# Kernel tuning notes

Measured on AMD Instinct MI355X. Metric: run time of the kernel, lower is better.

The kernel has to match this reference:

```python
import jax, jax.numpy as jnp
import numpy as np

B, T_SRC, T_TGT = 2048, 32, 32
D = 512            # d_model
D_SRC, D_TGT = 100, 80
L = 2              # n_layers


def setup_inputs() -> dict:
    key = jax.random.key(0)
    ks = jax.random.split(key, 16)
    s = 1.0 / float(np.sqrt(D))  # torch LSTM init scale
    u = lambda k, shape: jax.random.uniform(k, shape, jnp.float32, -s, s)
    return {
        "src": jax.random.randint(ks[0], (B, T_SRC), 0, D_SRC, dtype=jnp.int32),
        "tgt": jax.random.randint(ks[1], (B, T_TGT), 0, D_TGT, dtype=jnp.int32),
        "enc_emb": jax.random.normal(ks[2], (D_SRC, D), jnp.float32),
        "dec_emb": jax.random.normal(ks[3], (D_TGT, D), jnp.float32),
        "enc_Wih": u(ks[4], (L, 4 * D, D)),
        "enc_Whh": u(ks[5], (L, 4 * D, D)),
        "enc_bih": u(ks[6], (L, 4 * D)),
        "enc_bhh": u(ks[7], (L, 4 * D)),
        "dec_Wih": u(ks[8], (L, 4 * D, D)),
        "dec_Whh": u(ks[9], (L, 4 * D, D)),
        "dec_bih": u(ks[10], (L, 4 * D)),
        "dec_bhh": u(ks[11], (L, 4 * D)),
        "post_W": u(ks[12], (D_TGT, D)),
        "post_b": u(ks[13], (D_TGT,)),
    }


def lstm_cell(x, h, c, Wih, Whh, bih, bhh):
    # PyTorch gate order: i, f, g, o
    gates = x @ Wih.T + bih + h @ Whh.T + bhh  # [B, 4D]
    i, f, g, o = jnp.split(gates, 4, axis=-1)
    c_new = jax.nn.sigmoid(f) * c + jax.nn.sigmoid(i) * jnp.tanh(g)
    h_new = jax.nn.sigmoid(o) * jnp.tanh(c_new)
    return h_new, c_new


def reference(src, tgt, enc_emb, dec_emb, enc_Wih, enc_Whh, enc_bih, enc_bhh,
              dec_Wih, dec_Whh, dec_bih, dec_bhh, post_W, post_b):
    # Eval-mode forward: dropout = identity, teacher forcing disabled
    # (tf = random() < ratio AND self.training is False at inference).
    n_layers = enc_Wih.shape[0]
    Bb = src.shape[0]
    Dm = enc_emb.shape[1]

    # ---- encoder: multi-layer LSTM over src embeddings ----
    x = enc_emb[src].swapaxes(0, 1)  # [T_src, B, D]
    hs, cs = [], []
    z = jnp.zeros((Bb, Dm), x.dtype)
    for l in range(n_layers):
        def step(carry, xt, l=l):
            h, c = carry
            h, c = lstm_cell(xt, h, c, enc_Wih[l], enc_Whh[l], enc_bih[l], enc_bhh[l])
            return (h, c), h
        (hT, cT), x = jax.lax.scan(step, (z, z), x)
        hs.append(hT)
        cs.append(cT)
    h0 = jnp.stack(hs)  # [L, B, D]
    c0 = jnp.stack(cs)  # [L, B, D]

    prev0 = dec_emb[tgt[:, 0]]  # [B, D]

    def dec_step(carry, _):
        h, c, prev = carry
        x = prev
        new_h, new_c = [], []
        for l in range(n_layers):
            hl, cl = lstm_cell(x, h[l], c[l], dec_Wih[l], dec_Whh[l], dec_bih[l], dec_bhh[l])
            new_h.append(hl)
            new_c.append(cl)
            x = hl
        logits = x @ post_W.T + post_b          # [B, d_tgt]
        pred = jnp.argmax(logits, axis=-1)       # [B]
        prev = dec_emb[pred]                     # [B, D]
        return (jnp.stack(new_h), jnp.stack(new_c), prev), logits

    _, out = jax.lax.scan(dec_step, (h0, c0, prev0), None, length=tgt.shape[1])
    return out.swapaxes(0, 1)  # [B, T_tgt, d_tgt]
```

## Files before the change

### kernel.cpp

```cpp
#include <hip/hip_runtime.h>
#include <hip/hip_bf16.h>

#define B_  2048
#define T_  32
#define D_  512
#define G_  2048
#define VT_ 80
#define BD  (B_ * D_)
#define LWE ((size_t)G_ * D_)

typedef _Float16 half8 __attribute__((ext_vector_type(8)));
typedef _Float16 half4_t __attribute__((ext_vector_type(4)));
typedef float    f32x4 __attribute__((ext_vector_type(4)));

static __device__ __forceinline__ float sigm(float x) {
    return 1.0f / (1.0f + expf(-x));
}

__global__ void zero_ws(int4* __restrict__ p, int n) {
    int i = blockIdx.x * blockDim.x + threadIdx.x;
    if (i < n) p[i] = int4{0, 0, 0, 0};
}
__global__ void init_pred(const int* __restrict__ tgt, int* __restrict__ pred) {
    int i = blockIdx.x * blockDim.x + threadIdx.x;
    if (i < B_) pred[i] = tgt[i * T_];
}

__global__ void split_weights(const float* __restrict__ s0, const float* __restrict__ s1,
                              const float* __restrict__ s2, const float* __restrict__ s3,
                              const float* __restrict__ s4, const float* __restrict__ s5,
                              _Float16* __restrict__ Wbase) {
    int g = blockIdx.x * blockDim.x + threadIdx.x;
    int mat = g >> 17;
    int rem = g & 131071;
    int np  = rem >> 6;
    int kq  = rem & 63;
    const float* src = (mat == 0) ? s0 : (mat == 1) ? s1 : (mat == 2) ? s2
                     : (mat == 3) ? s3 : (mat == 4) ? s4 : s5;
    int n = (np & 3) * D_ + (np >> 2);
    const float* sp = src + (size_t)n * D_ + kq * 8;
    float4 v0 = ((const float4*)sp)[0], v1 = ((const float4*)sp)[1];
    float x[8] = {v0.x, v0.y, v0.z, v0.w, v1.x, v1.y, v1.z, v1.w};
    _Float16 hi[8], lo[8];
    #pragma unroll
    for (int u = 0; u < 8; ++u) {
        hi[u] = (_Float16)x[u];
        lo[u] = (_Float16)(x[u] - (float)hi[u]);
    }
    int tile = (np >> 4) * 16 + (kq >> 2);
    int lane = (np & 15) | ((kq & 3) << 4);
    size_t e = (size_t)tile * 512 + (size_t)lane * 8;
    _Float16* Whi = Wbase + (size_t)mat * (2 * LWE);
    _Float16* Wlo = Whi + LWE;
    *(half8*)(Whi + e) = *(half8*)hi;
    *(half8*)(Wlo + e) = *(half8*)lo;
}

__global__ void split_postW(const float* __restrict__ pw,
                            _Float16* __restrict__ Ph, _Float16* __restrict__ Pl) {
    int g = blockIdx.x * blockDim.x + threadIdx.x;
    if (g >= VT_ * 64) return;
    int v = g >> 6, kq = g & 63;
    const float* sp = pw + (size_t)v * D_ + kq * 8;
    float4 v0 = ((const float4*)sp)[0], v1 = ((const float4*)sp)[1];
    float x[8] = {v0.x, v0.y, v0.z, v0.w, v1.x, v1.y, v1.z, v1.w};
    _Float16 hi[8], lo[8];
    #pragma unroll
    for (int u = 0; u < 8; ++u) {
        hi[u] = (_Float16)x[u];
        lo[u] = (_Float16)(x[u] - (float)hi[u]);
    }
    int tile = (v >> 4) * 16 + (kq >> 2);
    int lane = (v & 15) | ((kq & 3) << 4);
    size_t e = (size_t)tile * 512 + (size_t)lane * 8;
    *(half8*)(Ph + e) = *(half8*)hi;
    *(half8*)(Pl + e) = *(half8*)lo;
}

__global__ void perm_bias(const float* __restrict__ ebih, const float* __restrict__ ebhh,
                          const float* __restrict__ dbih, const float* __restrict__ dbhh,
                          float* __restrict__ biasP) {
    int i = blockIdx.x * blockDim.x + threadIdx.x;
    int cfg = i >> 11, np = i & 2047;
    int n = (np & 3) * D_ + (np >> 2);
    const float* bi = ((cfg < 2) ? ebih : dbih) + (cfg & 1) * G_;
    const float* bh = ((cfg < 2) ? ebhh : dbhh) + (cfg & 1) * G_;
    biasP[cfg * G_ + np] = bi[n] + bh[n];
}

__global__ __launch_bounds__(256) void compute_P(
    const float* __restrict__ enc_emb, const float* __restrict__ dec_emb,
    const float* __restrict__ encW0,   const float* __restrict__ decW0,
    float* __restrict__ P) {
    __shared__ float es[10][D_];
    __shared__ float part[4][64][10];
    int by = blockIdx.y;
    bool enc = (by < 10);
    int r0 = enc ? by * 10 : 100 + (by - 10) * 10;
    int s0 = enc ? by * 10 : (by - 10) * 10;
    const float* emb = enc ? enc_emb : dec_emb;
    const float* W   = enc ? encW0 : decW0;
    int tid = threadIdx.x;
    #pragma unroll
    for (int it = 0; it < 5; ++it) {
        int i4 = it * 256 + tid;
        int rr = i4 >> 7, cc = i4 & 127;
        ((float4*)es[rr])[cc] = ((const float4*)(emb + (size_t)(s0 + rr) * D_))[cc];
    }
    __syncthreads();
    int o   = tid & 63;
    int seg = tid >> 6;
    int np = blockIdx.x * 64 + o;
    int n = (np & 3) * D_ + (np >> 2);
    const float* wr = W + (size_t)n * D_ + seg * 128;
    float acc[10];
    #pragma unroll
    for (int rr = 0; rr < 10; ++rr) acc[rr] = 0.f;
    for (int k = 0; k < 128; k += 4) {
        float4 w4 = *(const float4*)(wr + k);
        int kb = seg * 128 + k;
        #pragma unroll
        for (int rr = 0; rr < 10; ++rr)
            acc[rr] += es[rr][kb] * w4.x + es[rr][kb+1] * w4.y
                     + es[rr][kb+2] * w4.z + es[rr][kb+3] * w4.w;
    }
    #pragma unroll
    for (int rr = 0; rr < 10; ++rr) part[seg][o][rr] = acc[rr];
    __syncthreads();
    for (int i = tid; i < 640; i += 256) {
        int o2 = i & 63, rr = i >> 6;
        P[(size_t)(r0 + rr) * G_ + blockIdx.x * 64 + o2] =
            (part[0][o2][rr] + part[1][o2][rr]) + (part[2][o2][rr] + part[3][o2][rr]);
    }
}

static __device__ __forceinline__ void load_chunk(
    const _Float16* __restrict__ Ah, const _Float16* __restrict__ Al,
    const _Float16* __restrict__ Wh, const _Float16* __restrict__ Wl,
    int afr, int wfr, int kc, int lane, half8* A8, half8* B8) {
    size_t lo8 = (size_t)lane * 8;
    #pragma unroll
    for (int i = 0; i < 4; ++i) {
        size_t off = (((size_t)(afr + i) * 16 + kc) << 9) + lo8;
        A8[i]     = *(const half8*)(Ah + off);
        A8[4 + i] = *(const half8*)(Al + off);
    }
    #pragma unroll
    for (int j = 0; j < 4; ++j) {
        size_t off = (((size_t)(wfr + j) * 16 + kc) << 9) + lo8;
        B8[j]     = *(const half8*)(Wh + off);
        B8[4 + j] = *(const half8*)(Wl + off);
    }
}
static __device__ __forceinline__ void mfma_chunk(
    const half8* A8, const half8* B8, f32x4 acc[4][4]) {
    #pragma unroll
    for (int i = 0; i < 4; ++i)
        #pragma unroll
        for (int j = 0; j < 4; ++j) {
            acc[i][j] = __builtin_amdgcn_mfma_f32_16x16x32_f16(A8[i], B8[j], acc[i][j], 0, 0, 0);
            acc[i][j] = __builtin_amdgcn_mfma_f32_16x16x32_f16(A8[i], B8[4 + j], acc[i][j], 0, 0, 0);
            acc[i][j] = __builtin_amdgcn_mfma_f32_16x16x32_f16(A8[4 + i], B8[j], acc[i][j], 0, 0, 0);
        }
}

struct CellJob {
    const _Float16 *a0h, *a0l, *w0h, *w0l;
    int kclo0, kchi0;
    const _Float16 *a1h, *a1l, *w1h, *w1l;
    int kclo1, kchi1;
    const float *biasP;
    const float *P;
    const int  *idx;
    int idx_stride, emb_rows;
    float *c_io;
    _Float16 *hh_out, *hl_out;
};

__global__ __launch_bounds__(512, 2) void lstm_cell_mfma(CellJob J0, CellJob J1) {
    const CellJob J = (blockIdx.z == 0) ? J0 : J1;
    __shared__ float gf[128][68];
    const int tid  = threadIdx.x;
    const int w    = tid >> 6;
    const int lane = tid & 63;
    const int g    = w >> 2;
    const int mw   = w & 3;
    const int bx   = blockIdx.x;
    const int m0   = blockIdx.y * 256;

    const _Float16* Ah = g ? J.a1h : J.a0h;
    const _Float16* Al = g ? J.a1l : J.a0l;
    const _Float16* Wh = g ? J.w1h : J.w0h;
    const _Float16* Wl = g ? J.w1l : J.w0l;
    const int kclo = g ? J.kclo1 : J.kclo0;
    const int kchi = g ? J.kchi1 : J.kchi0;

    const int afr = (m0 >> 4) + mw * 4;
    const int wfr = bx * 4;

    f32x4 acc[4][4];
    #pragma unroll
    for (int i = 0; i < 4; ++i)
        #pragma unroll
        for (int j = 0; j < 4; ++j) acc[i][j] = f32x4{0.f, 0.f, 0.f, 0.f};

    half8 A0[8], B0[8], A1[8], B1[8];
    load_chunk(Ah, Al, Wh, Wl, afr, wfr, kclo, lane, A0, B0);
    for (int kc = kclo; kc < kchi; kc += 2) {
        load_chunk(Ah, Al, Wh, Wl, afr, wfr, kc + 1, lane, A1, B1);
        mfma_chunk(A0, B0, acc);
        if (kc + 2 < kchi)
            load_chunk(Ah, Al, Wh, Wl, afr, wfr, kc + 2, lane, A0, B0);
        mfma_chunk(A1, B1, acc);
    }

    const int rbase = (lane >> 4) << 2;
    const int cbase = lane & 15;
    for (int p = 0; p < 2; ++p) {
        if (g == 0 && (mw >> 1) == p) {
            #pragma unroll
            for (int i = 0; i < 4; ++i) {
                int mrow = (mw & 1) * 64 + i * 16 + rbase;
                #pragma unroll
                for (int j = 0; j < 4; ++j) {
                    int nc = j * 16 + cbase;
                    #pragma unroll
                    for (int r = 0; r < 4; ++r)
                        gf[mrow + r][nc] = acc[i][j][r];
                }
            }
        }
        __syncthreads();
        if (g == 1 && (mw >> 1) == p) {
            #pragma unroll
            for (int i = 0; i < 4; ++i) {
                int mrow = (mw & 1) * 64 + i * 16 + rbase;
                #pragma unroll
                for (int j = 0; j < 4; ++j) {
                    int nc = j * 16 + cbase;
                    #pragma unroll
                    for (int r = 0; r < 4; ++r)
                        gf[mrow + r][nc] += acc[i][j][r];
                }
            }
        }
        __syncthreads();
        {
            int mr = tid >> 2, q = tid & 3;
            int mg = m0 + p * 128 + mr;
            const float4* brow = (const float4*)(J.biasP + (bx << 6));
            const float4* Pr = nullptr;
            if (J.P) {
                int s = J.idx[mg * J.idx_stride];
                s = min(max(s, 0), J.emb_rows - 1);
                Pr = (const float4*)(J.P + (size_t)s * G_ + (bx << 6));
            }
            float* crow = J.c_io + (size_t)mg * D_ + (bx << 4) + (q << 2);
            float4 cv = *(float4*)crow;
            _Float16 hh4[4], hl4[4];
            #pragma unroll
            for (int e = 0; e < 4; ++e) {
                int dl = (q << 2) + e;
                float4 g4 = *(float4*)&gf[mr][dl << 2];
                float4 b4 = brow[dl];
                float gi = g4.x + b4.x, gF = g4.y + b4.y;
                float gg = g4.z + b4.z, go = g4.w + b4.w;
                if (Pr) {
                    float4 p4 = Pr[dl];
                    gi += p4.x; gF += p4.y; gg += p4.z; go += p4.w;
                }
                float cc = (&cv.x)[e];
                float cn = sigm(gF) * cc + sigm(gi) * tanhf(gg);
                float hn = sigm(go) * tanhf(cn);
                (&cv.x)[e] = cn;
                _Float16 hH = (_Float16)hn;
                hh4[e] = hH;
                hl4[e] = (_Float16)(hn - (float)hH);
            }
            *(float4*)crow = cv;
            int kk = (bx << 4) + (q << 2);
            size_t hoff = ((size_t)((mg >> 4) * 16 + (kk >> 5)) << 9)
                        + (size_t)((mg & 15) | (((kk >> 3) & 3) << 4)) * 8
                        + ((q & 1) << 2);
            *(half4_t*)(J.hh_out + hoff) = *(half4_t*)hh4;
            *(half4_t*)(J.hl_out + hoff) = *(half4_t*)hl4;
        }
        __syncthreads();
    }
}

__global__ __launch_bounds__(128) void logits_mfma(
    const _Float16* __restrict__ Ah, const _Float16* __restrict__ Al,
    const _Float16* __restrict__ Bh, const _Float16* __restrict__ Bl,
    const float* __restrict__ postb, float* __restrict__ out,
    int t, int* __restrict__ pred) {
    __shared__ float gf2[64][85];
    __shared__ float pb[VT_];
    const int tid = threadIdx.x;
    const int w = tid >> 6;
    const int lane = tid & 63;
    const int m0 = blockIdx.x * 64;
    const int afr = blockIdx.x * 4;

    f32x4 acc[4][5];
    #pragma unroll
    for (int i = 0; i < 4; ++i)
        #pragma unroll
        for (int j = 0; j < 5; ++j) acc[i][j] = f32x4{0.f, 0.f, 0.f, 0.f};

    size_t lo8 = (size_t)lane * 8;
    for (int kc = w * 8; kc < w * 8 + 8; ++kc) {
        half8 A8[8], Bh8[5], Bl8[5];
        #pragma unroll
        for (int i = 0; i < 4; ++i) {
            size_t off = (((size_t)(afr + i) * 16 + kc) << 9) + lo8;
            A8[i]     = *(const half8*)(Ah + off);
            A8[4 + i] = *(const half8*)(Al + off);
        }
        #pragma unroll
        for (int j = 0; j < 5; ++j) {
            size_t off = (((size_t)(j * 16 + kc)) << 9) + lo8;
            Bh8[j] = *(const half8*)(Bh + off);
            Bl8[j] = *(const half8*)(Bl + off);
        }
        #pragma unroll
        for (int i = 0; i < 4; ++i)
            #pragma unroll
            for (int j = 0; j < 5; ++j) {
                acc[i][j] = __builtin_amdgcn_mfma_f32_16x16x32_f16(A8[i], Bh8[j], acc[i][j], 0, 0, 0);
                acc[i][j] = __builtin_amdgcn_mfma_f32_16x16x32_f16(A8[i], Bl8[j], acc[i][j], 0, 0, 0);
                acc[i][j] = __builtin_amdgcn_mfma_f32_16x16x32_f16(A8[4 + i], Bh8[j], acc[i][j], 0, 0, 0);
            }
    }

    if (tid < VT_) pb[tid] = postb[tid];
    const int quad = lane >> 4, c = lane & 15;
    if (w == 0) {
        #pragma unroll
        for (int i = 0; i < 4; ++i)
            #pragma unroll
            for (int j = 0; j < 5; ++j)
                #pragma unroll
                for (int r = 0; r < 4; ++r)
                    gf2[i * 16 + quad * 4 + r][j * 16 + c] = acc[i][j][r];
    }
    __syncthreads();
    if (w == 1) {
        #pragma unroll
        for (int i = 0; i < 4; ++i)
            #pragma unroll
            for (int j = 0; j < 5; ++j)
                #pragma unroll
                for (int r = 0; r < 4; ++r)
                    gf2[i * 16 + quad * 4 + r][j * 16 + c] += acc[i][j][r];
    }
    __syncthreads();
    if (tid < 64) {
        int r = tid;
        float best = -3.4e38f; int bi = 0;
        #pragma unroll
        for (int v = 0; v < VT_; ++v) {
            float x = gf2[r][v] + pb[v];
            if (x > best) { best = x; bi = v; }
        }
        pred[m0 + r] = bi;
        float* orow = out + (size_t)(m0 + r) * (T_ * VT_) + (size_t)t * VT_;
        #pragma unroll
        for (int v4 = 0; v4 < VT_ / 4; ++v4) {
            float4 g4 = *(float4*)&gf2[r][v4 * 4];
            float4 b4 = *(float4*)&pb[v4 * 4];
            float4 o4 = {g4.x + b4.x, g4.y + b4.y, g4.z + b4.z, g4.w + b4.w};
            *(float4*)(orow + v4 * 4) = o4;
        }
    }
}

extern "C" void kernel_launch(void* const* d_in, const int* in_sizes, int n_in,
                              void* d_out, int out_size, void* d_ws, size_t ws_size,
                              hipStream_t stream) {
    (void)in_sizes; (void)n_in; (void)out_size; (void)ws_size;

    const int*   src     = (const int*)d_in[0];
    const int*   tgt     = (const int*)d_in[1];
    const float* enc_emb = (const float*)d_in[2];
    const float* dec_emb = (const float*)d_in[3];
    const float* enc_Wih = (const float*)d_in[4];
    const float* enc_Whh = (const float*)d_in[5];
    const float* enc_bih = (const float*)d_in[6];
    const float* enc_bhh = (const float*)d_in[7];
    const float* dec_Wih = (const float*)d_in[8];
    const float* dec_Whh = (const float*)d_in[9];
    const float* dec_bih = (const float*)d_in[10];
    const float* dec_bhh = (const float*)d_in[11];
    const float* post_W  = (const float*)d_in[12];
    const float* post_b  = (const float*)d_in[13];

    char* wsb = (char*)d_ws;
    int*   pred  = (int*)wsb;
    float* biasB = (float*)(wsb + 16384);
    float* Ptab  = (float*)(wsb + 16384 + 32768);
    char*  zbase = wsb + 16384 + 32768 + 180 * G_ * 4;
    float* C0 = (float*)zbase;
    float* C1 = C0 + BD;
    _Float16* Hh00 = (_Float16*)(C1 + BD);
    _Float16* Hh10 = Hh00 + BD;
    _Float16* Hl00 = Hh10 + BD;
    _Float16* Hl10 = Hl00 + BD;
    _Float16* Hh01 = Hl10 + BD;
    _Float16* Hh11 = Hh01 + BD;
    _Float16* Hl01 = Hh11 + BD;
    _Float16* Hl11 = Hl01 + BD;
    _Float16* Wb   = Hl11 + BD;
    _Float16* PwH  = Wb + 6 * 2 * LWE;
    _Float16* PwL  = PwH + (size_t)VT_ * D_;

    _Float16* Hhi[2][2] = { { Hh00, Hh01 }, { Hh10, Hh11 } };
    _Float16* Hlo[2][2] = { { Hl00, Hl01 }, { Hl10, Hl11 } };
    float*    Cp[2]     = { C0, C1 };
    auto WP = [&](int m, int pl) { return Wb + (size_t)m * (2 * LWE) + (size_t)pl * LWE; };

    float* out = (float*)d_out;

    zero_ws<<<4096, 256, 0, stream>>>((int4*)zbase, (16 * 1024 * 1024) / 16);
    init_pred<<<8, 256, 0, stream>>>(tgt, pred);
    split_weights<<<3072, 256, 0, stream>>>(
        enc_Whh, enc_Wih + LWE, enc_Whh + LWE,
        dec_Whh, dec_Wih + LWE, dec_Whh + LWE, Wb);
    split_postW<<<20, 256, 0, stream>>>(post_W, PwH, PwL);
    perm_bias<<<32, 256, 0, stream>>>(enc_bih, enc_bhh, dec_bih, dec_bhh, biasB);
    {
        dim3 gP(32, 18);
        compute_P<<<gP, 256, 0, stream>>>(enc_emb, dec_emb, enc_Wih, dec_Wih, Ptab);
    }

    dim3 grid1(G_ / 64, B_ / 256, 1);
    dim3 grid2(G_ / 64, B_ / 256, 2);
    int c0 = 0, c1 = 0;

    auto mkL0 = [&](bool enc, const int* ix, int stride, int rows) {
        int m = enc ? 0 : 3;
        CellJob j;
        j.a0h = Hhi[0][c0]; j.a0l = Hlo[0][c0];
        j.w0h = WP(m, 0);   j.w0l = WP(m, 1);
        j.kclo0 = 0; j.kchi0 = 8;
        j.a1h = Hhi[0][c0]; j.a1l = Hlo[0][c0];
        j.w1h = WP(m, 0);   j.w1l = WP(m, 1);
        j.kclo1 = 8; j.kchi1 = 16;
        j.biasP = biasB + (enc ? 0 : 2) * G_;
        j.P = enc ? Ptab : Ptab + (size_t)100 * G_;
        j.idx = ix; j.idx_stride = stride; j.emb_rows = rows;
        j.c_io = Cp[0];
        j.hh_out = Hhi[0][c0 ^ 1]; j.hl_out = Hlo[0][c0 ^ 1];
        return j;
    };
    auto mkL1 = [&](bool enc) {
        int mi = enc ? 1 : 4, mh = enc ? 2 : 5;
        CellJob j;
        j.a0h = Hhi[0][c0]; j.a0l = Hlo[0][c0];
        j.w0h = WP(mi, 0);  j.w0l = WP(mi, 1);
        j.kclo0 = 0; j.kchi0 = 16;
        j.a1h = Hhi[1][c1]; j.a1l = Hlo[1][c1];
        j.w1h = WP(mh, 0);  j.w1l = WP(mh, 1);
        j.kclo1 = 0; j.kchi1 = 16;
        j.biasP = biasB + (enc ? 1 : 3) * G_;
        j.P = nullptr; j.idx = nullptr; j.idx_stride = 0; j.emb_rows = 0;
        j.c_io = Cp[1];
        j.hh_out = Hhi[1][c1 ^ 1]; j.hl_out = Hlo[1][c1 ^ 1];
        return j;
    };

    {
        CellJob j0 = mkL0(true, src + 0, T_, 100);
        lstm_cell_mfma<<<grid1, 512, 0, stream>>>(j0, j0);
        c0 ^= 1;
        for (int t = 0; t < T_ - 1; ++t) {
            CellJob jA = mkL1(true);
            CellJob jB = mkL0(true, src + t + 1, T_, 100);
            lstm_cell_mfma<<<grid2, 512, 0, stream>>>(jA, jB);
            c1 ^= 1; c0 ^= 1;
        }
        CellJob jZ = mkL1(true);
        lstm_cell_mfma<<<grid1, 512, 0, stream>>>(jZ, jZ);
        c1 ^= 1;
    }

    for (int t = 0; t < T_; ++t) {
        CellJob j0 = mkL0(false, pred, 1, VT_);
        lstm_cell_mfma<<<grid1, 512, 0, stream>>>(j0, j0);
        c0 ^= 1;
        CellJob j1 = mkL1(false);
        lstm_cell_mfma<<<grid1, 512, 0, stream>>>(j1, j1);
        c1 ^= 1;
        logits_mfma<<<32, 128, 0, stream>>>(
            Hhi[1][c1], Hlo[1][c1], PwH, PwL, post_b, out, t, pred);
    }
}
```

Baseline: 4.255 ms.

## Halve LSTM cell M-tile and split K four ways across warps

The LSTM cell kernel now covers 128 batch rows per block instead of 256, which doubles the grid. Its 8 warps are arranged as 2 M-subtiles by 4 K-groups rather than 4 by 2. Layer-0 cells split K=16 chunks into four ranges of 4, and layer-1 cells split into two phases with two K halves each. The partial sums are reduced through shared memory in four sequential accumulate steps, and the single-pass epilogue computes the LSTM nonlinearity. This raises parallelism and halves per-warp K loop length, but adds more LDS reduction passes and barriers, and weight tiles are re-read by twice as many blocks.

```diff
diff --git a/kernel.cpp b/kernel.cpp
--- a/kernel.cpp
+++ b/kernel.cpp
@@ -166,9 +166,8 @@
 
 struct CellJob {
     const _Float16 *a0h, *a0l, *w0h, *w0l;
-    int kclo0, kchi0;
     const _Float16 *a1h, *a1l, *w1h, *w1l;
-    int kclo1, kchi1;
+    int nph;
     const float *biasP;
     const float *P;
     const int  *idx;
@@ -183,17 +182,19 @@
     const int tid  = threadIdx.x;
     const int w    = tid >> 6;
     const int lane = tid & 63;
-    const int g    = w >> 2;
-    const int mw   = w & 3;
+    const int g    = w >> 1;
+    const int mw   = w & 1;
     const int bx   = blockIdx.x;
-    const int m0   = blockIdx.y * 256;
-
-    const _Float16* Ah = g ? J.a1h : J.a0h;
-    const _Float16* Al = g ? J.a1l : J.a0l;
-    const _Float16* Wh = g ? J.w1h : J.w0h;
-    const _Float16* Wl = g ? J.w1l : J.w0l;
-    const int kclo = g ? J.kclo1 : J.kclo0;
-    const int kchi = g ? J.kchi1 : J.kchi0;
+    const int m0   = blockIdx.y * 128;
+
+    int ph, kclo, kchi;
+    if (J.nph == 2) { ph = g >> 1; kclo = (g & 1) * 8; kchi = kclo + 8; }
+    else            { ph = 0;      kclo = g * 4;       kchi = kclo + 4; }
+
+    const _Float16* Ah = ph ? J.a1h : J.a0h;
+    const _Float16* Al = ph ? J.a1l : J.a0l;
+    const _Float16* Wh = ph ? J.w1h : J.w0h;
+    const _Float16* Wl = ph ? J.w1l : J.w0l;
 
     const int afr = (m0 >> 4) + mw * 4;
     const int wfr = bx * 4;
@@ -216,25 +217,26 @@
 
     const int rbase = (lane >> 4) << 2;
     const int cbase = lane & 15;
-    for (int p = 0; p < 2; ++p) {
-        if (g == 0 && (mw >> 1) == p) {
+    if (g == 0) {
+        #pragma unroll
+        for (int i = 0; i < 4; ++i) {
+            int mrow = mw * 64 + i * 16 + rbase;
+            #pragma unroll
+            for (int j = 0; j < 4; ++j) {
+                int nc = j * 16 + cbase;
+                #pragma unroll
+                for (int r = 0; r < 4; ++r)
+                    gf[mrow + r][nc] = acc[i][j][r];
+            }
+        }
+    }
+    __syncthreads();
+    #pragma unroll
+    for (int gg = 1; gg < 4; ++gg) {
+        if (g == gg) {
             #pragma unroll
             for (int i = 0; i < 4; ++i) {
-                int mrow = (mw & 1) * 64 + i * 16 + rbase;
-                #pragma unroll
-                for (int j = 0; j < 4; ++j) {
-                    int nc = j * 16 + cbase;
-                    #pragma unroll
-                    for (int r = 0; r < 4; ++r)
-                        gf[mrow + r][nc] = acc[i][j][r];
-                }
-            }
-        }
-        __syncthreads();
-        if (g == 1 && (mw >> 1) == p) {
-            #pragma unroll
-            for (int i = 0; i < 4; ++i) {
-                int mrow = (mw & 1) * 64 + i * 16 + rbase;
+                int mrow = mw * 64 + i * 16 + rbase;
                 #pragma unroll
                 for (int j = 0; j < 4; ++j) {
                     int nc = j * 16 + cbase;
@@ -245,47 +247,46 @@
             }
         }
         __syncthreads();
-        {
-            int mr = tid >> 2, q = tid & 3;
-            int mg = m0 + p * 128 + mr;
-            const float4* brow = (const float4*)(J.biasP + (bx << 6));
-            const float4* Pr = nullptr;
-            if (J.P) {
-                int s = J.idx[mg * J.idx_stride];
-                s = min(max(s, 0), J.emb_rows - 1);
-                Pr = (const float4*)(J.P + (size_t)s * G_ + (bx << 6));
+    }
+    {
+        int mr = tid >> 2, q = tid & 3;
+        int mg = m0 + mr;
+        const float4* brow = (const float4*)(J.biasP + (bx << 6));
+        const float4* Pr = nullptr;
+        if (J.P) {
+            int s = J.idx[mg * J.idx_stride];
+            s = min(max(s, 0), J.emb_rows - 1);
+            Pr = (const float4*)(J.P + (size_t)s * G_ + (bx << 6));
+        }
+        float* crow = J.c_io + (size_t)mg * D_ + (bx << 4) + (q << 2);
+        float4 cv = *(float4*)crow;
+        _Float16 hh4[4], hl4[4];
+        #pragma unroll
+        for (int e = 0; e < 4; ++e) {
+            int dl = (q << 2) + e;
+            float4 g4 = *(float4*)&gf[mr][dl << 2];
+            float4 b4 = brow[dl];
+            float gi = g4.x + b4.x, gF = g4.y + b4.y;
+            float gg = g4.z + b4.z, go = g4.w + b4.w;
+            if (Pr) {
+                float4 p4 = Pr[dl];
+                gi += p4.x; gF += p4.y; gg += p4.z; go += p4.w;
             }
-            float* crow = J.c_io + (size_t)mg * D_ + (bx << 4) + (q << 2);
-            float4 cv = *(float4*)crow;
-            _Float16 hh4[4], hl4[4];
-            #pragma unroll
-            for (int e = 0; e < 4; ++e) {
-                int dl = (q << 2) + e;
-                float4 g4 = *(float4*)&gf[mr][dl << 2];
-                float4 b4 = brow[dl];
-                float gi = g4.x + b4.x, gF = g4.y + b4.y;
-                float gg = g4.z + b4.z, go = g4.w + b4.w;
-                if (Pr) {
-                    float4 p4 = Pr[dl];
-                    gi += p4.x; gF += p4.y; gg += p4.z; go += p4.w;
-                }
-                float cc = (&cv.x)[e];
-                float cn = sigm(gF) * cc + sigm(gi) * tanhf(gg);
-                float hn = sigm(go) * tanhf(cn);
-                (&cv.x)[e] = cn;
-                _Float16 hH = (_Float16)hn;
-                hh4[e] = hH;
-                hl4[e] = (_Float16)(hn - (float)hH);
-            }
-            *(float4*)crow = cv;
-            int kk = (bx << 4) + (q << 2);
-            size_t hoff = ((size_t)((mg >> 4) * 16 + (kk >> 5)) << 9)
-                        + (size_t)((mg & 15) | (((kk >> 3) & 3) << 4)) * 8
-                        + ((q & 1) << 2);
-            *(half4_t*)(J.hh_out + hoff) = *(half4_t*)hh4;
-            *(half4_t*)(J.hl_out + hoff) = *(half4_t*)hl4;
-        }
-        __syncthreads();
+            float cc = (&cv.x)[e];
+            float cn = sigm(gF) * cc + sigm(gi) * tanhf(gg);
+            float hn = sigm(go) * tanhf(cn);
+            (&cv.x)[e] = cn;
+            _Float16 hH = (_Float16)hn;
+            hh4[e] = hH;
+            hl4[e] = (_Float16)(hn - (float)hH);
+        }
+        *(float4*)crow = cv;
+        int kk = (bx << 4) + (q << 2);
+        size_t hoff = ((size_t)((mg >> 4) * 16 + (kk >> 5)) << 9)
+                    + (size_t)((mg & 15) | (((kk >> 3) & 3) << 4)) * 8
+                    + ((q & 1) << 2);
+        *(half4_t*)(J.hh_out + hoff) = *(half4_t*)hh4;
+        *(half4_t*)(J.hl_out + hoff) = *(half4_t*)hl4;
     }
 }
 
@@ -433,8 +434,8 @@
         compute_P<<<gP, 256, 0, stream>>>(enc_emb, dec_emb, enc_Wih, dec_Wih, Ptab);
     }
 
-    dim3 grid1(G_ / 64, B_ / 256, 1);
-    dim3 grid2(G_ / 64, B_ / 256, 2);
+    dim3 grid1(G_ / 64, B_ / 128, 1);
+    dim3 grid2(G_ / 64, B_ / 128, 2);
     int c0 = 0, c1 = 0;
 
     auto mkL0 = [&](bool enc, const int* ix, int stride, int rows) {
@@ -442,10 +443,8 @@
         CellJob j;
         j.a0h = Hhi[0][c0]; j.a0l = Hlo[0][c0];
         j.w0h = WP(m, 0);   j.w0l = WP(m, 1);
-        j.kclo0 = 0; j.kchi0 = 8;
-        j.a1h = Hhi[0][c0]; j.a1l = Hlo[0][c0];
-        j.w1h = WP(m, 0);   j.w1l = WP(m, 1);
-        j.kclo1 = 8; j.kchi1 = 16;
+        j.a1h = nullptr; j.a1l = nullptr; j.w1h = nullptr; j.w1l = nullptr;
+        j.nph = 1;
         j.biasP = biasB + (enc ? 0 : 2) * G_;
         j.P = enc ? Ptab : Ptab + (size_t)100 * G_;
         j.idx = ix; j.idx_stride = stride; j.emb_rows = rows;
@@ -458,10 +457,9 @@
         CellJob j;
         j.a0h = Hhi[0][c0]; j.a0l = Hlo[0][c0];
         j.w0h = WP(mi, 0);  j.w0l = WP(mi, 1);
-        j.kclo0 = 0; j.kchi0 = 16;
         j.a1h = Hhi[1][c1]; j.a1l = Hlo[1][c1];
         j.w1h = WP(mh, 0);  j.w1l = WP(mh, 1);
-        j.kclo1 = 0; j.kchi1 = 16;
+        j.nph = 2;
         j.biasP = biasB + (enc ? 1 : 3) * G_;
         j.P = nullptr; j.idx = nullptr; j.idx_stride = 0; j.emb_rows = 0;
         j.c_io = Cp[1];
```

New measurement: 4.759 ms. 11.8% more time.
